# Performance work log

Measured on AMD Instinct MI355X. Metric: run time of the kernel, lower is better.

Reference implementation:

```python
import jax, jax.numpy as jnp
import numpy as np

B, T, C = 2, 2048, 2048
H, KV, D = 16, 4, 128
G = H // KV  # kv groups
THETA = 10000.0


def setup_inputs() -> dict:
    key = jax.random.key(0)
    ks = jax.random.split(key, 5)
    x = jax.random.normal(ks[0], (B, T, C), dtype=jnp.float32)
    wq = jax.random.normal(ks[1], (H * D, C), dtype=jnp.float32) * 0.02
    wk = jax.random.normal(ks[2], (KV * D, C), dtype=jnp.float32) * 0.02
    wv = jax.random.normal(ks[3], (KV * D, C), dtype=jnp.float32) * 0.02
    wo = jax.random.normal(ks[4], (H * D, C), dtype=jnp.float32).T * 0.02  # [C, H*D] stored as [out,in]
    wo = jnp.asarray(wo)
    # rotary frequencies: freqs_cis = exp(i * t * theta^{-2j/D}) for j in [0, D/2)
    inv_freq = 1.0 / (THETA ** (jnp.arange(0, D, 2, dtype=jnp.float32) / D))  # [D/2]
    angles = jnp.arange(T, dtype=jnp.float32)[:, None] * inv_freq[None, :]    # [T, D/2]
    freqs_cos = jnp.cos(angles)
    freqs_sin = jnp.sin(angles)
    # additive causal mask [1,1,T,T]
    mask = jnp.where(jnp.tril(jnp.ones((T, T), dtype=bool)), 0.0, -1e9).astype(jnp.float32)[None, None]
    return {"x": x, "wq": wq, "wk": wk, "wv": wv, "wo": wo,
            "freqs_cos": freqs_cos, "freqs_sin": freqs_sin, "mask": mask}


def _apply_rope(t, cos, sin):
    # t: [B, T, nH, D]; cos/sin: [T, D/2]
    th = t.reshape(*t.shape[:-1], D // 2, 2)
    t0, t1 = th[..., 0], th[..., 1]
    c = cos[None, :, None, :]
    s = sin[None, :, None, :]
    o0 = t0 * c - t1 * s
    o1 = t0 * s + t1 * c
    return jnp.stack([o0, o1], axis=-1).reshape(t.shape)


def reference(x, wq, wk, wv, wo, freqs_cos, freqs_sin, mask):
    Bx, Tx, Cx = x.shape
    xq = (x @ wq.T).reshape(Bx, Tx, H, D)
    xk = (x @ wk.T).reshape(Bx, Tx, KV, D)
    xv = (x @ wv.T).reshape(Bx, Tx, KV, D)
    xq = _apply_rope(xq, freqs_cos, freqs_sin)
    xk = _apply_rope(xk, freqs_cos, freqs_sin)
    # GQA: repeat_interleave KV heads to match query heads
    xk = jnp.repeat(xk, G, axis=2)  # [B, T, H, D]
    xv = jnp.repeat(xv, G, axis=2)
    # [B, H, T, D]
    xq = xq.transpose(0, 2, 1, 3)
    xk = xk.transpose(0, 2, 1, 3)
    xv = xv.transpose(0, 2, 1, 3)
    scores = jnp.einsum('bhqd,bhkd->bhqk', xq, xk) / jnp.sqrt(jnp.float32(D))
    scores = scores + mask
    probs = jax.nn.softmax(scores.astype(jnp.float32), axis=-1).astype(xq.dtype)
    out = jnp.einsum('bhqk,bhkd->bhqd', probs, xv)
    out = out.transpose(0, 2, 1, 3).reshape(Bx, Tx, H * D)
    return out @ wo.T
```

## Files before the change

### kernel.cpp

```cpp
#include <hip/hip_runtime.h>
#include <hip/hip_bf16.h>

typedef __bf16 bf16_t;
typedef __bf16 bf16x8 __attribute__((ext_vector_type(8)));
typedef __bf16 bf16x4 __attribute__((ext_vector_type(4)));
typedef float f32x4 __attribute__((ext_vector_type(4)));
typedef float f32x16 __attribute__((ext_vector_type(16)));

#define SCALE_Q2 0.12752518895325724f

__device__ __forceinline__ void gload_lds16(const void* g, void* l) {
  __builtin_amdgcn_global_load_lds(
      (const __attribute__((address_space(1))) void*)g,
      (__attribute__((address_space(3))) void*)l, 16, 0, 0);
}

__global__ __launch_bounds__(256) void cvt_f32_bf16(
    const float* __restrict__ src, bf16_t* __restrict__ dst, int n4) {
  int i = blockIdx.x * 256 + threadIdx.x;
  const int stride = gridDim.x * 256;
  for (; i < n4; i += stride) {
    f32x4 v = *reinterpret_cast<const f32x4*>(src + (size_t)i * 4);
    bf16x4 r;
    r[0] = (bf16_t)v[0]; r[1] = (bf16_t)v[1];
    r[2] = (bf16_t)v[2]; r[3] = (bf16_t)v[3];
    *reinterpret_cast<bf16x4*>(dst + (size_t)i * 4) = r;
  }
}

__global__ __launch_bounds__(256) void cvt_qkvw(
    const float* __restrict__ wq, const float* __restrict__ wk,
    const float* __restrict__ wv, bf16_t* __restrict__ dst) {
  const int i = blockIdx.x * 256 + threadIdx.x;
  const int e = i * 4;
  const float* src;
  if (e < 4194304) src = wq + e;
  else if (e < 5242880) src = wk + (e - 4194304);
  else src = wv + (e - 5242880);
  f32x4 v = *reinterpret_cast<const f32x4*>(src);
  bf16x4 r;
  r[0] = (bf16_t)v[0]; r[1] = (bf16_t)v[1];
  r[2] = (bf16_t)v[2]; r[3] = (bf16_t)v[3];
  *reinterpret_cast<bf16x4*>(dst + e) = r;
}

template <typename OutT>
__global__ __launch_bounds__(256) void gemm_bt(
    const bf16_t* __restrict__ A, const bf16_t* __restrict__ W,
    OutT* __restrict__ C, int M, int N, int K) {
  __shared__ bf16_t As[128 * 32];
  __shared__ bf16_t Ws[128 * 32];
  const int tid = threadIdx.x;
  const int lane = tid & 63;
  const int wid = tid >> 6;
  const int wr = wid >> 1, wc = wid & 1;
  const int l15 = lane & 15, lg = lane >> 4;
  const int r0 = blockIdx.y * 128;
  const int c0 = blockIdx.x * 128;

  f32x4 acc[4][4];
#pragma unroll
  for (int mi = 0; mi < 4; ++mi)
#pragma unroll
    for (int ni = 0; ni < 4; ++ni)
#pragma unroll
      for (int j = 0; j < 4; ++j) acc[mi][ni][j] = 0.f;

  for (int k0 = 0; k0 < K; k0 += 32) {
#pragma unroll
    for (int s = 0; s < 2; ++s) {
      const int chunk = wid * 2 + s;
      const int eoff = (chunk * 64 + lane) * 8;
      const int r = eoff >> 5, c = eoff & 31;
      gload_lds16(A + (size_t)(r0 + r) * K + k0 + c, (char*)As + chunk * 1024);
      gload_lds16(W + (size_t)(c0 + r) * K + k0 + c, (char*)Ws + chunk * 1024);
    }
    __syncthreads();
    bf16x8 af[4], wf[4];
#pragma unroll
    for (int mi = 0; mi < 4; ++mi)
      af[mi] = *reinterpret_cast<const bf16x8*>(
          &As[(wr * 64 + mi * 16 + l15) * 32 + lg * 8]);
#pragma unroll
    for (int ni = 0; ni < 4; ++ni)
      wf[ni] = *reinterpret_cast<const bf16x8*>(
          &Ws[(wc * 64 + ni * 16 + l15) * 32 + lg * 8]);
#pragma unroll
    for (int mi = 0; mi < 4; ++mi)
#pragma unroll
      for (int ni = 0; ni < 4; ++ni)
        acc[mi][ni] = __builtin_amdgcn_mfma_f32_16x16x32_bf16(
            af[mi], wf[ni], acc[mi][ni], 0, 0, 0);
    __syncthreads();
  }

#pragma unroll
  for (int mi = 0; mi < 4; ++mi)
#pragma unroll
    for (int ni = 0; ni < 4; ++ni)
#pragma unroll
      for (int j = 0; j < 4; ++j) {
        const int row = r0 + wr * 64 + mi * 16 + lg * 4 + j;
        const int col = c0 + wc * 64 + ni * 16 + l15;
        const float v = acc[mi][ni][j];
        if constexpr (__is_same(OutT, float))
          C[(size_t)row * N + col] = v;
        else
          C[(size_t)row * N + col] = (bf16_t)v;
      }
}

__global__ __launch_bounds__(256) void rope_layout(
    const bf16_t* __restrict__ qkv, const float* __restrict__ fc,
    const float* __restrict__ fs, bf16_t* __restrict__ Qr,
    bf16_t* __restrict__ Kr) {
  const int n = blockIdx.x;
  const int b = n >> 11, t = n & 2047;
  const int tid = threadIdx.x;
  const bf16_t* row = qkv + (size_t)n * 3072;

#pragma unroll
  for (int i = 0; i < 4; ++i) {
    const int p = i * 256 + tid;
    const int h = p >> 6, j = p & 63;
    const float t0 = (float)row[h * 128 + 2 * j];
    const float t1 = (float)row[h * 128 + 2 * j + 1];
    const float c = fc[t * 64 + j], s = fs[t * 64 + j];
    const size_t dst = ((size_t)(b * 16 + h) * 2048 + t) * 128 + 2 * j;
    Qr[dst] = (bf16_t)((t0 * c - t1 * s) * SCALE_Q2);
    Qr[dst + 1] = (bf16_t)((t0 * s + t1 * c) * SCALE_Q2);
  }
  {
    const int kvh = tid >> 6, j = tid & 63;
    const float t0 = (float)row[2048 + kvh * 128 + 2 * j];
    const float t1 = (float)row[2048 + kvh * 128 + 2 * j + 1];
    const float c = fc[t * 64 + j], s = fs[t * 64 + j];
    const size_t dst = ((size_t)(b * 4 + kvh) * 2048 + t) * 128 + 2 * j;
    Kr[dst] = (bf16_t)(t0 * c - t1 * s);
    Kr[dst + 1] = (bf16_t)(t0 * s + t1 * c);
  }
}

__global__ __launch_bounds__(256) void v_trans(
    const bf16_t* __restrict__ qkv, bf16_t* __restrict__ Vt) {
  __shared__ bf16_t L[64][68];
  const int bid = blockIdx.x;
  const int tt = bid & 31;
  const int dt2 = (bid >> 5) & 1;
  const int bk = bid >> 6;
  const int b = bk >> 2, kvh = bk & 3;
  const int t0 = tt * 64, d0 = dt2 * 64;
  const int r = threadIdx.x >> 4;
  const int c4 = (threadIdx.x & 15) * 4;

#pragma unroll
  for (int it = 0; it < 4; ++it) {
    const int tl = r + it * 16;
    const int tp = (tl & ~15) |
                   ((tl & 3) | ((tl & 4) << 1) | ((tl & 8) >> 1));
    const bf16_t* src = qkv + (size_t)(b * 2048 + t0 + tl) * 3072 + 2560 +
                        kvh * 128 + d0 + c4;
    *reinterpret_cast<bf16x4*>(&L[tp][c4]) =
        *reinterpret_cast<const bf16x4*>(src);
  }
  __syncthreads();
#pragma unroll
  for (int it = 0; it < 4; ++it) {
    const int dr = r + it * 16;
    bf16x4 v;
#pragma unroll
    for (int j = 0; j < 4; ++j) v[j] = L[c4 + j][dr];
    *reinterpret_cast<bf16x4*>(Vt + ((size_t)bk * 128 + d0 + dr) * 2048 +
                               t0 + c4) = v;
  }
}

__global__ __launch_bounds__(256, 2) void attn_fwd(
    const bf16_t* __restrict__ Qr, const bf16_t* __restrict__ Kr,
    const bf16_t* __restrict__ Vt, bf16_t* __restrict__ Oout) {
  __shared__ __align__(16) bf16_t Klds[2][96 * 128];
  const int tid = threadIdx.x;
  const int lane = tid & 63, w = tid >> 6;
  const int l31 = lane & 31, hi = lane >> 5;
  const int sidx = blockIdx.x >> 5;
  const int hb = blockIdx.x & 31;
  const int h = hb & 15, b = hb >> 4;
  const int kvh = h >> 2;
  const int st = (sidx < 8) ? (15 - sidx) : (sidx - 8);

  const bf16_t* Kbase = Kr + ((size_t)(b * 4 + kvh) * 2048) * 128;
  const bf16_t* Vbase = Vt + ((size_t)(b * 4 + kvh) * 128) * 2048;

  const int qbw = st * 128 + w * 32;
  const bf16_t* Qbase = Qr + ((size_t)(b * 16 + h) * 2048 + qbw + l31) * 128;

  auto STAGE = [&](bf16_t* dst, int kt) {
    const int k0s = kt * 96;
#pragma unroll
    for (int i = 0; i < 6; ++i) {
      const int c = i * 256 + tid;
      const int row = c >> 4;
      const int col = c & 15;
      const int scol = col ^ (row & 15);
      int gr = k0s + row;
      if (gr > 2047) gr = 2047;
      gload_lds16(Kbase + (size_t)gr * 128 + scol * 8, dst + c * 8);
    }
  };

  STAGE(&Klds[0][0], 0);

  bf16x8 qf[8];
#pragma unroll
  for (int dt = 0; dt < 8; ++dt)
    qf[dt] = *reinterpret_cast<const bf16x8*>(Qbase + dt * 16 + hi * 8);

  f32x16 o[4];
#pragma unroll
  for (int d = 0; d < 4; ++d)
#pragma unroll
    for (int r = 0; r < 16; ++r) o[d][r] = 0.f;
  float lsum = 0.f;

  const int nt = ((st + 1) * 128 + 95) / 96;
  int cur = 0;
  for (int kt = 0; kt < nt; ++kt) {
    const int k0 = kt * 96;

    __syncthreads();
    if (kt + 1 < nt) STAGE(&Klds[cur ^ 1][0], kt + 1);

    if (k0 <= qbw) {
      const bool do1 = (k0 + 32 <= qbw);
      const bool do2 = (k0 + 64 <= qbw);
      const char* KB = (const char*)&Klds[cur][0];

      auto QK = [&](f32x16& sv, int qi) __attribute__((always_inline)) {
#pragma unroll
        for (int r = 0; r < 16; ++r) sv[r] = 0.f;
#pragma unroll
        for (int dt = 0; dt < 8; ++dt) {
          const int boff = (qi * 32 + l31) * 256 +
                           ((dt * 32 + hi * 16) ^ ((l31 & 15) << 4));
          bf16x8 ka = *reinterpret_cast<const bf16x8*>(KB + boff);
          sv = __builtin_amdgcn_mfma_f32_32x32x16_bf16(ka, qf[dt], sv, 0, 0, 0);
        }
      };
      auto VLOADQ = [&](bf16x8 buf[4], int qi, int kc)
          __attribute__((always_inline)) {
#pragma unroll
        for (int dtile = 0; dtile < 4; ++dtile)
          buf[dtile] = *reinterpret_cast<const bf16x8*>(
              Vbase + (size_t)(dtile * 32 + l31) * 2048 + k0 + qi * 32 +
              kc * 16 + hi * 8);
      };
      auto SMPV = [&](const f32x16& sv, bool diag, bf16x8 va0[4],
                      bf16x8 va1[4]) __attribute__((always_inline)) {
        float p[16];
#pragma unroll
        for (int r = 0; r < 16; ++r) {
          float e = exp2f(sv[r]);
          if (diag) {
            const int crow = (r & 3) + 8 * (r >> 2) + 4 * hi;
            if (crow > l31) e = 0.f;
          }
          p[r] = e;
        }
        const float t0 = (p[0] + p[1]) + (p[2] + p[3]);
        const float t1 = (p[4] + p[5]) + (p[6] + p[7]);
        const float t2 = (p[8] + p[9]) + (p[10] + p[11]);
        const float t3 = (p[12] + p[13]) + (p[14] + p[15]);
        lsum += (t0 + t1) + (t2 + t3);
#pragma unroll
        for (int kc = 0; kc < 2; ++kc) {
          unsigned int u0, u1, u2, u3;
          asm("v_cvt_pk_bf16_f32 %0, %1, %2" : "=v"(u0)
              : "v"(p[8 * kc + 0]), "v"(p[8 * kc + 1]));
          asm("v_cvt_pk_bf16_f32 %0, %1, %2" : "=v"(u1)
              : "v"(p[8 * kc + 2]), "v"(p[8 * kc + 3]));
          asm("v_cvt_pk_bf16_f32 %0, %1, %2" : "=v"(u2)
              : "v"(p[8 * kc + 4]), "v"(p[8 * kc + 5]));
          asm("v_cvt_pk_bf16_f32 %0, %1, %2" : "=v"(u3)
              : "v"(p[8 * kc + 6]), "v"(p[8 * kc + 7]));
          union { unsigned int u[4]; bf16x8 v; } pb;
          pb.u[0] = u0; pb.u[1] = u1; pb.u[2] = u2; pb.u[3] = u3;
          bf16x8* va = kc ? va1 : va0;
          __builtin_amdgcn_s_setprio(1);
#pragma unroll
          for (int dtile = 0; dtile < 4; ++dtile)
            o[dtile] = __builtin_amdgcn_mfma_f32_32x32x16_bf16(
                va[dtile], pb.v, o[dtile], 0, 0, 0);
          __builtin_amdgcn_s_setprio(0);
        }
      };

      bf16x8 vaA[4], vaB[4];
      VLOADQ(vaA, 0, 0);
      VLOADQ(vaB, 0, 1);

      f32x16 sA, sB;
      __builtin_amdgcn_s_setprio(1);
      QK(sA, 0);
      if (do1) QK(sB, 1);
      __builtin_amdgcn_s_setprio(0);

      SMPV(sA, k0 == qbw, vaA, vaB);
      if (do1) {
        VLOADQ(vaA, 1, 0);
        VLOADQ(vaB, 1, 1);
        SMPV(sB, k0 + 32 == qbw, vaA, vaB);
        if (do2) {
          VLOADQ(vaA, 2, 0);
          VLOADQ(vaB, 2, 1);
          __builtin_amdgcn_s_setprio(1);
          QK(sA, 2);
          __builtin_amdgcn_s_setprio(0);
          SMPV(sA, k0 + 64 == qbw, vaA, vaB);
        }
      }
    }
    cur ^= 1;
  }

  const float ltot = lsum + __shfl_xor(lsum, 32);
  const float inv = 1.f / ltot;
  bf16_t* Obase = Oout + ((size_t)b * 2048 + qbw + l31) * 2048 + h * 128;
#pragma unroll
  for (int dtile = 0; dtile < 4; ++dtile)
#pragma unroll
    for (int g = 0; g < 4; ++g) {
      bf16x4 stv;
#pragma unroll
      for (int j = 0; j < 4; ++j)
        stv[j] = (bf16_t)(o[dtile][g * 4 + j] * inv);
      *reinterpret_cast<bf16x4*>(Obase + dtile * 32 + 8 * g + 4 * hi) = stv;
    }
}

extern "C" void kernel_launch(void* const* d_in, const int* in_sizes, int n_in,
                              void* d_out, int out_size, void* d_ws,
                              size_t ws_size, hipStream_t stream) {
  const float* x  = (const float*)d_in[0];
  const float* wq = (const float*)d_in[1];
  const float* wk = (const float*)d_in[2];
  const float* wv = (const float*)d_in[3];
  const float* wo = (const float*)d_in[4];
  const float* fc = (const float*)d_in[5];
  const float* fs = (const float*)d_in[6];
  float* out = (float*)d_out;

  char* ws = (char*)d_ws;
  bf16_t* xb      = (bf16_t*)(ws + 0);
  bf16_t* wqkv    = (bf16_t*)(ws + 16777216);
  bf16_t* wo_b    = (bf16_t*)(ws + 29360128);
  bf16_t* qkv     = (bf16_t*)(ws + 37748736);
  bf16_t* Qr      = (bf16_t*)(ws + 62914560);
  bf16_t* Kr      = (bf16_t*)(ws + 79691776);
  bf16_t* Vt      = (bf16_t*)(ws + 83886080);
  bf16_t* attn_o  = xb;

  const int M = 4096;

  cvt_f32_bf16<<<2048, 256, 0, stream>>>(x, xb, 2097152);
  cvt_qkvw<<<6144, 256, 0, stream>>>(wq, wk, wv, wqkv);
  cvt_f32_bf16<<<1024, 256, 0, stream>>>(wo, wo_b, 1048576);

  gemm_bt<bf16_t><<<dim3(3072 / 128, M / 128), 256, 0, stream>>>(
      xb, wqkv, qkv, M, 3072, 2048);

  rope_layout<<<4096, 256, 0, stream>>>(qkv, fc, fs, Qr, Kr);
  v_trans<<<512, 256, 0, stream>>>(qkv, Vt);

  attn_fwd<<<512, 256, 0, stream>>>(Qr, Kr, Vt, attn_o);

  gemm_bt<float><<<dim3(2048 / 128, M / 128), 256, 0, stream>>>(
      attn_o, wo_b, out, M, 2048, 2048);
}
```

Measured before the change: 239.0 us.

## Split attention KV range across two wave groups and merge partials via LDS

Attention blocks now use 512 threads: two halves of four waves each process alternating 64-key tiles for the same 128 query rows, staging two K tiles per iteration into a 4-deep LDS buffer. At the end, the second half writes its partial O accumulators and row sums to LDS, and the first half adds them and normalizes. This doubles the wave-level parallelism per query block to shorten the serial KV loop, at the cost of an extra LDS reduction, more register pressure with the 512-thread launch bounds, and dropping the 96-wide tile schedule.

```diff
diff --git a/kernel.cpp b/kernel.cpp
--- a/kernel.cpp
+++ b/kernel.cpp
@@ -175,12 +175,14 @@
   }
 }
 
-__global__ __launch_bounds__(256, 2) void attn_fwd(
+__global__ __launch_bounds__(512, 2) void attn_fwd(
     const bf16_t* __restrict__ Qr, const bf16_t* __restrict__ Kr,
     const bf16_t* __restrict__ Vt, bf16_t* __restrict__ Oout) {
-  __shared__ __align__(16) bf16_t Klds[2][96 * 128];
+  __shared__ __align__(16) bf16_t Klds[4][64 * 128];
+  __shared__ float LS[4][64];
   const int tid = threadIdx.x;
-  const int lane = tid & 63, w = tid >> 6;
+  const int lane = tid & 63, W = tid >> 6;
+  const int qw = W & 3, half = W >> 2;
   const int l31 = lane & 31, hi = lane >> 5;
   const int sidx = blockIdx.x >> 5;
   const int hb = blockIdx.x & 31;
@@ -191,24 +193,23 @@
   const bf16_t* Kbase = Kr + ((size_t)(b * 4 + kvh) * 2048) * 128;
   const bf16_t* Vbase = Vt + ((size_t)(b * 4 + kvh) * 128) * 2048;
 
-  const int qbw = st * 128 + w * 32;
+  const int qbw = st * 128 + qw * 32;
   const bf16_t* Qbase = Qr + ((size_t)(b * 16 + h) * 2048 + qbw + l31) * 128;
 
-  auto STAGE = [&](bf16_t* dst, int kt) {
-    const int k0s = kt * 96;
-#pragma unroll
-    for (int i = 0; i < 6; ++i) {
-      const int c = i * 256 + tid;
+  auto STAGE = [&](bf16_t* dst, int t) {
+    const int k0s = t * 64;
+#pragma unroll
+    for (int i = 0; i < 2; ++i) {
+      const int c = i * 512 + tid;
       const int row = c >> 4;
       const int col = c & 15;
       const int scol = col ^ (row & 15);
-      int gr = k0s + row;
-      if (gr > 2047) gr = 2047;
-      gload_lds16(Kbase + (size_t)gr * 128 + scol * 8, dst + c * 8);
+      gload_lds16(Kbase + (size_t)(k0s + row) * 128 + scol * 8, dst + c * 8);
     }
   };
 
   STAGE(&Klds[0][0], 0);
+  STAGE(&Klds[1][0], 1);
 
   bf16x8 qf[8];
 #pragma unroll
@@ -222,18 +223,18 @@
     for (int r = 0; r < 16; ++r) o[d][r] = 0.f;
   float lsum = 0.f;
 
-  const int nt = ((st + 1) * 128 + 95) / 96;
-  int cur = 0;
-  for (int kt = 0; kt < nt; ++kt) {
-    const int k0 = kt * 96;
-
+  const int nw = st + 1;
+  for (int j = 0; j < nw; ++j) {
     __syncthreads();
-    if (kt + 1 < nt) STAGE(&Klds[cur ^ 1][0], kt + 1);
-
+    if (j + 1 < nw) {
+      STAGE(&Klds[(2 * j + 2) & 3][0], 2 * j + 2);
+      STAGE(&Klds[(2 * j + 3) & 3][0], 2 * j + 3);
+    }
+    const int t = 2 * j + half;
+    const int k0 = t * 64;
     if (k0 <= qbw) {
       const bool do1 = (k0 + 32 <= qbw);
-      const bool do2 = (k0 + 64 <= qbw);
-      const char* KB = (const char*)&Klds[cur][0];
+      const char* KB = (const char*)&Klds[t & 3][0];
 
       auto QK = [&](f32x16& sv, int qi) __attribute__((always_inline)) {
 #pragma unroll
@@ -309,32 +310,43 @@
         VLOADQ(vaA, 1, 0);
         VLOADQ(vaB, 1, 1);
         SMPV(sB, k0 + 32 == qbw, vaA, vaB);
-        if (do2) {
-          VLOADQ(vaA, 2, 0);
-          VLOADQ(vaB, 2, 1);
-          __builtin_amdgcn_s_setprio(1);
-          QK(sA, 2);
-          __builtin_amdgcn_s_setprio(0);
-          SMPV(sA, k0 + 64 == qbw, vaA, vaB);
-        }
       }
     }
-    cur ^= 1;
-  }
-
-  const float ltot = lsum + __shfl_xor(lsum, 32);
-  const float inv = 1.f / ltot;
-  bf16_t* Obase = Oout + ((size_t)b * 2048 + qbw + l31) * 2048 + h * 128;
-#pragma unroll
-  for (int dtile = 0; dtile < 4; ++dtile)
-#pragma unroll
-    for (int g = 0; g < 4; ++g) {
-      bf16x4 stv;
-#pragma unroll
-      for (int j = 0; j < 4; ++j)
-        stv[j] = (bf16_t)(o[dtile][g * 4 + j] * inv);
-      *reinterpret_cast<bf16x4*>(Obase + dtile * 32 + 8 * g + 4 * hi) = stv;
-    }
+  }
+
+  __syncthreads();
+  float* F = (float*)&Klds[0][0];
+  if (half == 1) {
+#pragma unroll
+    for (int dtile = 0; dtile < 4; ++dtile)
+#pragma unroll
+      for (int r = 0; r < 16; ++r)
+        F[(dtile * 16 + r) * 256 + qw * 64 + lane] = o[dtile][r];
+    LS[qw][lane] = lsum;
+  }
+  __syncthreads();
+  if (half == 0) {
+    lsum += LS[qw][lane];
+#pragma unroll
+    for (int dtile = 0; dtile < 4; ++dtile)
+#pragma unroll
+      for (int r = 0; r < 16; ++r)
+        o[dtile][r] += F[(dtile * 16 + r) * 256 + qw * 64 + lane];
+
+    const float ltot = lsum + __shfl_xor(lsum, 32);
+    const float inv = 1.f / ltot;
+    bf16_t* Obase = Oout + ((size_t)b * 2048 + qbw + l31) * 2048 + h * 128;
+#pragma unroll
+    for (int dtile = 0; dtile < 4; ++dtile)
+#pragma unroll
+      for (int g = 0; g < 4; ++g) {
+        bf16x4 stv;
+#pragma unroll
+        for (int j2 = 0; j2 < 4; ++j2)
+          stv[j2] = (bf16_t)(o[dtile][g * 4 + j2] * inv);
+        *reinterpret_cast<bf16x4*>(Obase + dtile * 32 + 8 * g + 4 * hi) = stv;
+      }
+  }
 }
 
 extern "C" void kernel_launch(void* const* d_in, const int* in_sizes, int n_in,
@@ -371,7 +383,7 @@
   rope_layout<<<4096, 256, 0, stream>>>(qkv, fc, fs, Qr, Kr);
   v_trans<<<512, 256, 0, stream>>>(qkv, Vt);
 
-  attn_fwd<<<512, 256, 0, stream>>>(Qr, Kr, Vt, attn_o);
+  attn_fwd<<<512, 512, 0, stream>>>(Qr, Kr, Vt, attn_o);
 
   gemm_bt<float><<<dim3(2048 / 128, M / 128), 256, 0, stream>>>(
       attn_o, wo_b, out, M, 2048, 2048);
```

Result: slower. 261.7 us (+9.5%).
